# Optimization experiments

Measured on AMD Instinct MI355X. Metric: run time of the kernel, lower is better.

Reference implementation:

```python
import jax, jax.numpy as jnp
import numpy as np

MARGIN = 1.0


def setup_inputs() -> dict:
    key = jax.random.key(0)
    k1, k2 = jax.random.split(key)
    B, C = 2048, 32000
    scores = jax.random.normal(k1, (B, C), dtype=jnp.float32)
    targets = jax.random.randint(k2, (B,), 0, C, dtype=jnp.int64)
    return {"scores": scores, "targets": targets}


def reference(scores, targets):
    B, C = scores.shape
    dt = scores.dtype
    # rank of ground-truth under descending sort (1-based), matches torch argsort(descending)+argmax
    sorted_idx = jnp.argsort(-scores, axis=-1)                      # [B, C]
    rank = jnp.argmax(sorted_idx == targets[:, None], axis=-1) + 1  # [B]
    # harmonic-number rank weights H(rank) via on-device cumulative sum of reciprocals
    harm = jnp.cumsum(1.0 / jnp.arange(1, C + 1, dtype=dt))         # [C], harm[k-1] = H(k)
    rank_weights = jax.lax.stop_gradient(harm[rank - 1])            # [B]
    # hinge loss: sum_y relu-masked (margin*1[y!=y_n] + s(x,y) - s(x,y_n))
    mask = (targets[:, None] != jnp.arange(C)[None, :]).astype(dt)  # [B, C]
    gt_scores = jnp.take_along_axis(scores, targets[:, None], axis=1)  # [B, 1]
    l = (mask * MARGIN + scores - gt_scores) * mask                 # [B, C]
    mask_pos = (l > 0).astype(dt)
    hinge = jnp.sum(l * mask_pos, axis=-1)                          # [B]
    n_pos = jnp.sum(mask_pos, axis=-1) + 1e-7                       # [B]
    loss = rank_weights / n_pos * hinge
    return jnp.mean(loss)
```

## Files before the change

### kernel.cpp

```cpp
#include <hip/hip_runtime.h>

#define B_DIM 2048
#define C_DIM 32000
#define MARGIN 1.0f
#define NTHREADS 256

__device__ __forceinline__ float waveReduceSum(float v) {
    #pragma unroll
    for (int off = 32; off > 0; off >>= 1)
        v += __shfl_down(v, off, 64);
    return v;
}

__global__ __launch_bounds__(NTHREADS) void row_loss_kernel(
        const float* __restrict__ scores,
        const int* __restrict__ targets,
        float* __restrict__ row_loss) {
    const int b = blockIdx.x;
    const int tid = threadIdx.x;
    const int lane = tid & 63;
    const int wave = tid >> 6;

    const float* row = scores + (size_t)b * C_DIM;

    __shared__ float s_gt;
    if (tid == 0) s_gt = row[targets[b]];
    __syncthreads();
    const float gt = s_gt;
    const float thr = gt - MARGIN;

    int   cntG = 0;
    float cntP = 0.f;
    float sumH = 0.f;

    const float4* row4 = (const float4*)row;
    const int n4 = C_DIM / 4;
    for (int i = tid; i < n4; i += NTHREADS) {
        float4 v = row4[i];
        cntG += (v.x > gt); cntG += (v.y > gt); cntG += (v.z > gt); cntG += (v.w > gt);
        if (v.x > thr) { cntP += 1.f; sumH += (MARGIN + v.x - gt); }
        if (v.y > thr) { cntP += 1.f; sumH += (MARGIN + v.y - gt); }
        if (v.z > thr) { cntP += 1.f; sumH += (MARGIN + v.z - gt); }
        if (v.w > thr) { cntP += 1.f; sumH += (MARGIN + v.w - gt); }
    }

    __shared__ float red[4][4];
    float cg = waveReduceSum((float)cntG);
    float cp = waveReduceSum(cntP);
    float sh = waveReduceSum(sumH);
    if (lane == 0) { red[wave][0] = cg; red[wave][1] = cp; red[wave][2] = sh; }
    __syncthreads();

    __shared__ int   s_rank;
    __shared__ float s_np, s_sh;
    if (tid == 0) {
        float tg = 0.f, tp = 0.f, th = 0.f;
        #pragma unroll
        for (int w = 0; w < 4; ++w) { tg += red[w][0]; tp += red[w][1]; th += red[w][2]; }
        s_rank = (int)tg + 1;
        s_np   = tp - 1.0f;
        s_sh   = th - 1.0f;
    }
    __syncthreads();

    const int rank = s_rank;
    float h = 0.f;
    for (int k = tid + 1; k <= rank; k += NTHREADS) h += 1.0f / (float)k;
    h = waveReduceSum(h);
    if (lane == 0) red[wave][3] = h;
    __syncthreads();

    if (tid == 0) {
        float H = red[0][3] + red[1][3] + red[2][3] + red[3][3];
        float loss = H / (s_np + 1e-7f) * s_sh;
        row_loss[b] = loss;
    }
}

__global__ __launch_bounds__(NTHREADS) void mean_kernel(
        const float* __restrict__ row_loss, float* __restrict__ out) {
    const int tid = threadIdx.x;
    float s = 0.f;
    for (int i = tid; i < B_DIM; i += NTHREADS) s += row_loss[i];
    s = waveReduceSum(s);
    __shared__ float red[4];
    const int lane = tid & 63, wave = tid >> 6;
    if (lane == 0) red[wave] = s;
    __syncthreads();
    if (tid == 0) out[0] = (red[0] + red[1] + red[2] + red[3]) * (1.0f / (float)B_DIM);
}

extern "C" void kernel_launch(void* const* d_in, const int* in_sizes, int n_in,
                              void* d_out, int out_size, void* d_ws, size_t ws_size,
                              hipStream_t stream) {
    const float* scores  = (const float*)d_in[0];
    const int*   targets = (const int*)d_in[1];
    float* row_loss = (float*)d_ws;
    float* out      = (float*)d_out;

    row_loss_kernel<<<B_DIM, NTHREADS, 0, stream>>>(scores, targets, row_loss);
    mean_kernel<<<1, NTHREADS, 0, stream>>>(row_loss, out);
}
```

Before: 371.1 us.

## Use asymptotic harmonic formula, unroll row scan, and drop extra block syncs

Replaces the per-block parallel harmonic-number summation up to rank with an asymptotic expansion (log n + gamma + 1/2n - 1/12n^2) for large ranks, with a serial sum for small ones. This removes a loop, a reduction and two barriers per row. The row scan is rewritten as a fixed-count loop that issues four float4 loads per iteration, with branchless hinge accumulation using fmaxf and integer counters. Each thread now reads the ground-truth score directly instead of going through shared memory. The approximation and the use of integer counters may cause small numeric differences from the reference.

Result: faster. 357.4 us (-3.7%).

```diff
diff --git a/kernel.cpp b/kernel.cpp
--- a/kernel.cpp
+++ b/kernel.cpp
@@ -1,4 +1,5 @@
 #include <hip/hip_runtime.h>
+#include <math.h>
 
 #define B_DIM 2048
 #define C_DIM 32000
@@ -12,6 +13,15 @@
     return v;
 }
 
+__device__ __forceinline__ void acc4(float4 v, float gt, float thr,
+                                     int& cntG, int& cntP, float& sumH) {
+    cntG += (v.x > gt); cntG += (v.y > gt); cntG += (v.z > gt); cntG += (v.w > gt);
+    float dx = v.x - thr, dy = v.y - thr, dz = v.z - thr, dw = v.w - thr;
+    cntP += (dx > 0.f); cntP += (dy > 0.f); cntP += (dz > 0.f); cntP += (dw > 0.f);
+    sumH += fmaxf(dx, 0.f); sumH += fmaxf(dy, 0.f);
+    sumH += fmaxf(dz, 0.f); sumH += fmaxf(dw, 0.f);
+}
+
 __global__ __launch_bounds__(NTHREADS) void row_loss_kernel(
         const float* __restrict__ scores,
         const int* __restrict__ targets,
@@ -21,59 +31,69 @@
     const int lane = tid & 63;
     const int wave = tid >> 6;
 
-    const float* row = scores + (size_t)b * C_DIM;
+    const float* __restrict__ row = scores + (size_t)b * C_DIM;
 
-    __shared__ float s_gt;
-    if (tid == 0) s_gt = row[targets[b]];
-    __syncthreads();
-    const float gt = s_gt;
+    const int tgt  = targets[b];
+    const float gt = row[tgt];
     const float thr = gt - MARGIN;
 
     int   cntG = 0;
-    float cntP = 0.f;
+    int   cntP = 0;
     float sumH = 0.f;
 
-    const float4* row4 = (const float4*)row;
-    const int n4 = C_DIM / 4;
-    for (int i = tid; i < n4; i += NTHREADS) {
-        float4 v = row4[i];
-        cntG += (v.x > gt); cntG += (v.y > gt); cntG += (v.z > gt); cntG += (v.w > gt);
-        if (v.x > thr) { cntP += 1.f; sumH += (MARGIN + v.x - gt); }
-        if (v.y > thr) { cntP += 1.f; sumH += (MARGIN + v.y - gt); }
-        if (v.z > thr) { cntP += 1.f; sumH += (MARGIN + v.z - gt); }
-        if (v.w > thr) { cntP += 1.f; sumH += (MARGIN + v.w - gt); }
+    const float4* __restrict__ row4 = (const float4*)row;
+    const float4* p = row4 + tid;
+    #pragma unroll 1
+    for (int k = 0; k < 7; ++k) {
+        float4 a0 = p[0];
+        float4 a1 = p[NTHREADS];
+        float4 a2 = p[2 * NTHREADS];
+        float4 a3 = p[3 * NTHREADS];
+        acc4(a0, gt, thr, cntG, cntP, sumH);
+        acc4(a1, gt, thr, cntG, cntP, sumH);
+        acc4(a2, gt, thr, cntG, cntP, sumH);
+        acc4(a3, gt, thr, cntG, cntP, sumH);
+        p += 4 * NTHREADS;
+    }
+    {
+        float4 a0 = p[0];
+        float4 a1 = p[NTHREADS];
+        float4 a2 = p[2 * NTHREADS];
+        acc4(a0, gt, thr, cntG, cntP, sumH);
+        acc4(a1, gt, thr, cntG, cntP, sumH);
+        acc4(a2, gt, thr, cntG, cntP, sumH);
+    }
+    if (tid < 64) {
+        float4 a0 = row4[7936 + tid];
+        acc4(a0, gt, thr, cntG, cntP, sumH);
     }
 
-    __shared__ float red[4][4];
     float cg = waveReduceSum((float)cntG);
-    float cp = waveReduceSum(cntP);
+    float cp = waveReduceSum((float)cntP);
     float sh = waveReduceSum(sumH);
+
+    __shared__ float red[4][3];
     if (lane == 0) { red[wave][0] = cg; red[wave][1] = cp; red[wave][2] = sh; }
     __syncthreads();
 
-    __shared__ int   s_rank;
-    __shared__ float s_np, s_sh;
     if (tid == 0) {
         float tg = 0.f, tp = 0.f, th = 0.f;
         #pragma unroll
         for (int w = 0; w < 4; ++w) { tg += red[w][0]; tp += red[w][1]; th += red[w][2]; }
-        s_rank = (int)tg + 1;
-        s_np   = tp - 1.0f;
-        s_sh   = th - 1.0f;
-    }
-    __syncthreads();
+        int rank = (int)tg + 1;
+        float n_pos = tp - 1.0f;
+        float hinge = th - 1.0f;
 
-    const int rank = s_rank;
-    float h = 0.f;
-    for (int k = tid + 1; k <= rank; k += NTHREADS) h += 1.0f / (float)k;
-    h = waveReduceSum(h);
-    if (lane == 0) red[wave][3] = h;
-    __syncthreads();
-
-    if (tid == 0) {
-        float H = red[0][3] + red[1][3] + red[2][3] + red[3][3];
-        float loss = H / (s_np + 1e-7f) * s_sh;
-        row_loss[b] = loss;
+        float H;
+        if (rank >= 40) {
+            float n = (float)rank;
+            float inv = 1.0f / n;
+            H = logf(n) + 0.57721566f + 0.5f * inv - (1.0f / 12.0f) * inv * inv;
+        } else {
+            H = 0.f;
+            for (int k = 1; k <= rank; ++k) H += 1.0f / (float)k;
+        }
+        row_loss[b] = H / (n_pos + 1e-7f) * hinge;
     }
 }
 
```
